# Kernel tuning notes

Hardware: AMD Instinct MI355X
Metric: run time of the kernel (lower is better)

## Reference

```python
import jax, jax.numpy as jnp
import numpy as np

N_NODES = 100000
N_EDGES = 1600000
IN_CH, HID, N_CLS = 768, 256, 8


def setup_inputs() -> dict:
    key = jax.random.key(0)
    k1, k2, k3, k4 = jax.random.split(key, 4)
    x = jax.random.normal(k1, (N_NODES, IN_CH), dtype=jnp.float32)
    edge_index = jax.random.randint(k2, (2, N_EDGES), 0, N_NODES, dtype=jnp.int64)
    # Glorot-ish init scaled for stability
    W1 = jax.random.normal(k3, (IN_CH, HID), dtype=jnp.float32) * (1.0 / np.sqrt(IN_CH))
    b1 = jnp.zeros((HID,), dtype=jnp.float32)
    W2 = jax.random.normal(k4, (HID, N_CLS), dtype=jnp.float32) * (1.0 / np.sqrt(HID))
    b2 = jnp.zeros((N_CLS,), dtype=jnp.float32)
    return {"x": x, "edge_index": edge_index, "W1": W1, "b1": b1, "W2": W2, "b2": b2}


def _gcn_norm(edge_index, num_nodes):
    # Add self-loops (PyG GCNConv default) and compute symmetric normalization.
    loops = jnp.arange(num_nodes, dtype=edge_index.dtype)
    row = jnp.concatenate([edge_index[0], loops])  # source nodes
    col = jnp.concatenate([edge_index[1], loops])  # target nodes
    ones = jnp.ones(col.shape[0], dtype=jnp.float32)
    deg = jax.ops.segment_sum(ones, col, num_segments=num_nodes)
    dinv = jnp.where(deg > 0, jax.lax.rsqrt(deg), 0.0)
    norm = dinv[row] * dinv[col]  # [E + N]
    return row, col, norm


def _gcn_conv(x, row, col, norm, W, b):
    h = x @ W                      # [N, out] dense transform first (out <= in)
    msg = h[row] * norm[:, None]    # gather + scale, [E+N, out]
    agg = jax.ops.segment_sum(msg, col, num_segments=x.shape[0])  # scatter-add
    return agg + b


def reference(x, edge_index, W1, b1, W2, b2):
    row, col, norm = _gcn_norm(edge_index, x.shape[0])
    h = _gcn_conv(x, row, col, norm, W1, b1)
    h = jax.nn.relu(h)
    # dropout is identity at eval (training=False)
    out = _gcn_conv(h, row, col, norm, W2, b2)
    return out
```

## Files before the change

kernel.cpp:

```cpp
#include <hip/hip_runtime.h>


#define NN 100000
#define NE 1600000
#define INC 768
#define HID 256
#define NCLS 8
#define NBLK 391

typedef short bf16x8 __attribute__((ext_vector_type(8)));
typedef float f32x4 __attribute__((ext_vector_type(4)));

__device__ __forceinline__ unsigned short f2bf(float f) {
  unsigned int u = __float_as_uint(f);
  unsigned int r = (u + 0x7FFFu + ((u >> 16) & 1u)) >> 16;
  return (unsigned short)r;
}
__device__ __forceinline__ float bf2f(unsigned short h) {
  return __uint_as_float(((unsigned int)h) << 16);
}

__global__ __launch_bounds__(256) void k_count(const int* __restrict__ ei, int* __restrict__ cnt) {
  int e = blockIdx.x * 256 + threadIdx.x;
  if (e < NE) atomicAdd(&cnt[ei[NE + e]], 1);
}

__global__ __launch_bounds__(256) void k_scan1(const int* __restrict__ cnt, int* __restrict__ bsum,
                                               float* __restrict__ dinv) {
  __shared__ int s[256];
  int i = blockIdx.x * 256 + threadIdx.x;
  int v = (i < NN) ? cnt[i] : 0;
  if (i < NN) dinv[i] = rsqrtf((float)v + 1.0f);
  s[threadIdx.x] = v;
  __syncthreads();
#pragma unroll
  for (int off = 128; off > 0; off >>= 1) {
    if (threadIdx.x < off) s[threadIdx.x] += s[threadIdx.x + off];
    __syncthreads();
  }
  if (threadIdx.x == 0) bsum[blockIdx.x] = s[0];
}
__global__ __launch_bounds__(512) void k_scan2(const int* __restrict__ bsum, int* __restrict__ boff,
                                               int* __restrict__ rowptr) {
  __shared__ int s[512];
  int tid = threadIdx.x;
  int v = (tid < NBLK) ? bsum[tid] : 0;
  s[tid] = v;
  __syncthreads();
#pragma unroll
  for (int off = 1; off < 512; off <<= 1) {
    int t = (tid >= off) ? s[tid - off] : 0;
    __syncthreads();
    s[tid] += t;
    __syncthreads();
  }
  if (tid < NBLK) boff[tid] = s[tid] - v;
  if (tid == NBLK - 1) rowptr[NN] = s[tid];
}
__global__ __launch_bounds__(256) void k_scan3(const int* __restrict__ cnt, const int* __restrict__ boff,
                                               int* __restrict__ rowptr, int* __restrict__ cursor) {
  __shared__ int s[256];
  int i = blockIdx.x * 256 + threadIdx.x;
  int v = (i < NN) ? cnt[i] : 0;
  s[threadIdx.x] = v;
  __syncthreads();
#pragma unroll
  for (int off = 1; off < 256; off <<= 1) {
    int t = (threadIdx.x >= off) ? s[threadIdx.x - off] : 0;
    __syncthreads();
    s[threadIdx.x] += t;
    __syncthreads();
  }
  if (i < NN) {
    int e = boff[blockIdx.x] + s[threadIdx.x] - v;
    rowptr[i] = e;
    cursor[i] = e;
  }
}
__global__ __launch_bounds__(256) void k_fill(const int* __restrict__ ei, const float* __restrict__ dinv,
                                              int* __restrict__ cursor, int2* __restrict__ epk) {
  int e = blockIdx.x * 256 + threadIdx.x;
  if (e >= NE) return;
  int r = ei[e];
  int c = ei[NE + e];
  float w = dinv[r] * dinv[c];
  int pos = atomicAdd(&cursor[c], 1);
  epk[pos] = make_int2(r, __float_as_int(w));
}

__global__ __launch_bounds__(256) void k_w1t(const float* __restrict__ W1, unsigned short* __restrict__ w1t) {
  int t = blockIdx.x * 256 + threadIdx.x;
  if (t >= INC * HID) return;
  int k = t / HID, n = t % HID;
  w1t[n * INC + k] = f2bf(W1[t]);
}

__global__ __launch_bounds__(512) void k_gemm1(const float* __restrict__ x,
                                               const unsigned short* __restrict__ w1t,
                                               unsigned short* __restrict__ h1) {
  __shared__ char smem[49152];
  unsigned short* As = (unsigned short*)smem;
  unsigned short* Bs = (unsigned short*)(smem + 16384);
  const int tid = threadIdx.x;
  const int lane = tid & 63;
  const int wid = tid >> 6;
  const int wm = wid >> 2;
  const int wn = wid & 3;
  const long bm = blockIdx.x;

  const int ar0 = tid >> 3, as7 = tid & 7;
  const int ar1 = (tid + 512) >> 3;
  long arow0 = bm * 128 + ar0; if (arow0 > NN - 1) arow0 = NN - 1;
  long arow1 = bm * 128 + ar1; if (arow1 > NN - 1) arow1 = NN - 1;
  const float* gA0 = x + arow0 * INC + as7 * 8;
  const float* gA1 = x + arow1 * INC + as7 * 8;
  const int aoff0 = (ar0 << 7) | ((as7 ^ (ar0 & 7)) << 4);
  const int aoff1 = (ar1 << 7) | ((as7 ^ (ar1 & 7)) << 4);

  f32x4 acc[4][4];
#pragma unroll
  for (int m = 0; m < 4; m++)
#pragma unroll
    for (int n = 0; n < 4; n++) acc[m][n] = (f32x4){0.f, 0.f, 0.f, 0.f};

  float4 fa00, fa01, fa10, fa11;
  uint4 rb0, rb1, rb2, rb3;

#define LOAD_AB(KT)                                                        \
  do {                                                                     \
    fa00 = *(const float4*)(gA0 + (KT));                                   \
    fa01 = *(const float4*)(gA0 + (KT) + 4);                               \
    fa10 = *(const float4*)(gA1 + (KT));                                   \
    fa11 = *(const float4*)(gA1 + (KT) + 4);                               \
    rb0 = *(const uint4*)(w1t + (long)(tid >> 3) * INC + (KT) + (tid & 7) * 8);            \
    rb1 = *(const uint4*)(w1t + (long)((tid + 512) >> 3) * INC + (KT) + (tid & 7) * 8);    \
    rb2 = *(const uint4*)(w1t + (long)((tid + 1024) >> 3) * INC + (KT) + (tid & 7) * 8);   \
    rb3 = *(const uint4*)(w1t + (long)((tid + 1536) >> 3) * INC + (KT) + (tid & 7) * 8);   \
  } while (0)

  LOAD_AB(0);

  for (int kt = 0; kt < INC; kt += 64) {
    {
      union { unsigned short us[8]; uint4 v; } u;
      u.us[0] = f2bf(fa00.x); u.us[1] = f2bf(fa00.y); u.us[2] = f2bf(fa00.z); u.us[3] = f2bf(fa00.w);
      u.us[4] = f2bf(fa01.x); u.us[5] = f2bf(fa01.y); u.us[6] = f2bf(fa01.z); u.us[7] = f2bf(fa01.w);
      *(uint4*)((char*)As + aoff0) = u.v;
      u.us[0] = f2bf(fa10.x); u.us[1] = f2bf(fa10.y); u.us[2] = f2bf(fa10.z); u.us[3] = f2bf(fa10.w);
      u.us[4] = f2bf(fa11.x); u.us[5] = f2bf(fa11.y); u.us[6] = f2bf(fa11.z); u.us[7] = f2bf(fa11.w);
      *(uint4*)((char*)As + aoff1) = u.v;
    }
    {
      int r0 = tid >> 3, s7 = tid & 7;
      *(uint4*)((char*)Bs + ((r0 << 7) | ((s7 ^ (r0 & 7)) << 4))) = rb0;
      int r1 = (tid + 512) >> 3;
      *(uint4*)((char*)Bs + ((r1 << 7) | ((s7 ^ (r1 & 7)) << 4))) = rb1;
      int r2 = (tid + 1024) >> 3;
      *(uint4*)((char*)Bs + ((r2 << 7) | ((s7 ^ (r2 & 7)) << 4))) = rb2;
      int r3 = (tid + 1536) >> 3;
      *(uint4*)((char*)Bs + ((r3 << 7) | ((s7 ^ (r3 & 7)) << 4))) = rb3;
    }
    __syncthreads();
    if (kt + 64 < INC) LOAD_AB(kt + 64);
#pragma unroll
    for (int half = 0; half < 2; half++) {
      bf16x8 af[4], bff[4];
      int j = (half << 2) + (lane >> 4);
#pragma unroll
      for (int m = 0; m < 4; m++) {
        int row = wm * 64 + m * 16 + (lane & 15);
        int off = (row << 7) | ((j ^ (row & 7)) << 4);
        af[m] = *(const bf16x8*)((const char*)As + off);
      }
#pragma unroll
      for (int n = 0; n < 4; n++) {
        int row = wn * 64 + n * 16 + (lane & 15);
        int off = (row << 7) | ((j ^ (row & 7)) << 4);
        bff[n] = *(const bf16x8*)((const char*)Bs + off);
      }
#pragma unroll
      for (int m = 0; m < 4; m++)
#pragma unroll
        for (int n = 0; n < 4; n++)
          acc[m][n] = __builtin_amdgcn_mfma_f32_16x16x32_bf16(af[m], bff[n], acc[m][n], 0, 0, 0);
    }
    __syncthreads();
  }
#undef LOAD_AB

  unsigned short* Os = (unsigned short*)smem;
#pragma unroll
  for (int chunk = 0; chunk < 2; chunk++) {
    if (wm == chunk) {
#pragma unroll
      for (int m = 0; m < 4; m++)
#pragma unroll
        for (int n = 0; n < 4; n++) {
          int lrow = m * 16 + ((lane >> 4) << 2);
          int lcol = wn * 64 + n * 16 + (lane & 15);
#pragma unroll
          for (int r = 0; r < 4; r++)
            Os[(lrow + r) * 264 + lcol] = f2bf(acc[m][n][r]);
        }
    }
    __syncthreads();
    {
      int r = tid >> 3, s = tid & 7;
      long grow = bm * 128 + chunk * 64 + r;
      if (grow < NN) {
        unsigned short* dst = h1 + grow * HID;
#pragma unroll
        for (int i = 0; i < 4; i++) {
          int seg = s + i * 8;
          *(uint4*)(dst + seg * 8) = *(const uint4*)((const char*)Os + (long)r * 528 + seg * 16);
        }
      }
    }
    __syncthreads();
  }
}

__global__ __launch_bounds__(256) void k_agg1(const unsigned short* __restrict__ h1,
                                              const float* __restrict__ dinv,
                                              const int* __restrict__ rowptr,
                                              const int2* __restrict__ epk,
                                              const float* __restrict__ b1,
                                              const float* __restrict__ W2,
                                              float* __restrict__ h2) {
  int w = (int)((blockIdx.x * 256 + threadIdx.x) >> 6);
  int lane = threadIdx.x & 63;
  if (w >= NN) return;
  float di = dinv[w];
  int c4 = lane << 2;
  const unsigned short* hb = h1 + c4;
  ushort4 hv = *(const ushort4*)(hb + (long)w * HID);
  float self = di * di;
  float a0 = self * bf2f(hv.x), a1 = self * bf2f(hv.y);
  float a2 = self * bf2f(hv.z), a3 = self * bf2f(hv.w);
  int e = rowptr[w], e1 = rowptr[w + 1];
  if ((e & 1) && e < e1) {
    int2 q = epk[e];
    float ws = __int_as_float(q.y);
    ushort4 g = *(const ushort4*)(hb + (long)q.x * HID);
    a0 += ws * bf2f(g.x); a1 += ws * bf2f(g.y);
    a2 += ws * bf2f(g.z); a3 += ws * bf2f(g.w);
    e++;
  }
  for (; e + 8 <= e1; e += 8) {
    uint4 p0 = *(const uint4*)(epk + e);
    uint4 p1 = *(const uint4*)(epk + e + 2);
    uint4 p2 = *(const uint4*)(epk + e + 4);
    uint4 p3 = *(const uint4*)(epk + e + 6);
    ushort4 g0 = *(const ushort4*)(hb + (long)(int)p0.x * HID);
    ushort4 g1 = *(const ushort4*)(hb + (long)(int)p0.z * HID);
    ushort4 g2 = *(const ushort4*)(hb + (long)(int)p1.x * HID);
    ushort4 g3 = *(const ushort4*)(hb + (long)(int)p1.z * HID);
    ushort4 g4 = *(const ushort4*)(hb + (long)(int)p2.x * HID);
    ushort4 g5 = *(const ushort4*)(hb + (long)(int)p2.z * HID);
    ushort4 g6 = *(const ushort4*)(hb + (long)(int)p3.x * HID);
    ushort4 g7 = *(const ushort4*)(hb + (long)(int)p3.z * HID);
    float w0 = __uint_as_float(p0.y), w1 = __uint_as_float(p0.w);
    float w2 = __uint_as_float(p1.y), w3 = __uint_as_float(p1.w);
    float w4 = __uint_as_float(p2.y), w5 = __uint_as_float(p2.w);
    float w6 = __uint_as_float(p3.y), w7 = __uint_as_float(p3.w);
    a0 += w0 * bf2f(g0.x) + w1 * bf2f(g1.x) + w2 * bf2f(g2.x) + w3 * bf2f(g3.x) +
          w4 * bf2f(g4.x) + w5 * bf2f(g5.x) + w6 * bf2f(g6.x) + w7 * bf2f(g7.x);
    a1 += w0 * bf2f(g0.y) + w1 * bf2f(g1.y) + w2 * bf2f(g2.y) + w3 * bf2f(g3.y) +
          w4 * bf2f(g4.y) + w5 * bf2f(g5.y) + w6 * bf2f(g6.y) + w7 * bf2f(g7.y);
    a2 += w0 * bf2f(g0.z) + w1 * bf2f(g1.z) + w2 * bf2f(g2.z) + w3 * bf2f(g3.z) +
          w4 * bf2f(g4.z) + w5 * bf2f(g5.z) + w6 * bf2f(g6.z) + w7 * bf2f(g7.z);
    a3 += w0 * bf2f(g0.w) + w1 * bf2f(g1.w) + w2 * bf2f(g2.w) + w3 * bf2f(g3.w) +
          w4 * bf2f(g4.w) + w5 * bf2f(g5.w) + w6 * bf2f(g6.w) + w7 * bf2f(g7.w);
  }
  for (; e + 2 <= e1; e += 2) {
    uint4 p = *(const uint4*)(epk + e);
    ushort4 g0 = *(const ushort4*)(hb + (long)(int)p.x * HID);
    ushort4 g1 = *(const ushort4*)(hb + (long)(int)p.z * HID);
    float w0 = __uint_as_float(p.y), w1 = __uint_as_float(p.w);
    a0 += w0 * bf2f(g0.x) + w1 * bf2f(g1.x);
    a1 += w0 * bf2f(g0.y) + w1 * bf2f(g1.y);
    a2 += w0 * bf2f(g0.z) + w1 * bf2f(g1.z);
    a3 += w0 * bf2f(g0.w) + w1 * bf2f(g1.w);
  }
  if (e < e1) {
    int2 q = epk[e];
    float ws = __int_as_float(q.y);
    ushort4 g = *(const ushort4*)(hb + (long)q.x * HID);
    a0 += ws * bf2f(g.x); a1 += ws * bf2f(g.y);
    a2 += ws * bf2f(g.z); a3 += ws * bf2f(g.w);
  }
  float4 bv = *(const float4*)(b1 + c4);
  float v0 = a0 + bv.x; v0 = v0 > 0.f ? v0 : 0.f;
  float v1 = a1 + bv.y; v1 = v1 > 0.f ? v1 : 0.f;
  float v2 = a2 + bv.z; v2 = v2 > 0.f ? v2 : 0.f;
  float v3 = a3 + bv.w; v3 = v3 > 0.f ? v3 : 0.f;
  const float4* wp = (const float4*)(W2 + ((long)c4 << 3));
  float4 r0a = wp[0], r0b = wp[1], r1a = wp[2], r1b = wp[3];
  float4 r2a = wp[4], r2b = wp[5], r3a = wp[6], r3b = wp[7];
  float p[8];
  p[0] = v0 * r0a.x + v1 * r1a.x + v2 * r2a.x + v3 * r3a.x;
  p[1] = v0 * r0a.y + v1 * r1a.y + v2 * r2a.y + v3 * r3a.y;
  p[2] = v0 * r0a.z + v1 * r1a.z + v2 * r2a.z + v3 * r3a.z;
  p[3] = v0 * r0a.w + v1 * r1a.w + v2 * r2a.w + v3 * r3a.w;
  p[4] = v0 * r0b.x + v1 * r1b.x + v2 * r2b.x + v3 * r3b.x;
  p[5] = v0 * r0b.y + v1 * r1b.y + v2 * r2b.y + v3 * r3b.y;
  p[6] = v0 * r0b.z + v1 * r1b.z + v2 * r2b.z + v3 * r3b.z;
  p[7] = v0 * r0b.w + v1 * r1b.w + v2 * r2b.w + v3 * r3b.w;
#pragma unroll
  for (int c = 0; c < 8; c++)
#pragma unroll
    for (int off = 1; off < 64; off <<= 1) p[c] += __shfl_xor(p[c], off, 64);
  if (lane < 8) {
    float o = p[0];
    o = (lane == 1) ? p[1] : o;
    o = (lane == 2) ? p[2] : o;
    o = (lane == 3) ? p[3] : o;
    o = (lane == 4) ? p[4] : o;
    o = (lane == 5) ? p[5] : o;
    o = (lane == 6) ? p[6] : o;
    o = (lane == 7) ? p[7] : o;
    h2[(long)w * NCLS + lane] = o;
  }
}

__global__ __launch_bounds__(256) void k_agg2(const float* __restrict__ h2,
                                              const float* __restrict__ dinv,
                                              const int* __restrict__ rowptr,
                                              const int2* __restrict__ epk,
                                              const float* __restrict__ b2,
                                              float* __restrict__ out) {
  long t = (long)blockIdx.x * 256 + threadIdx.x;
  long i = t >> 3;
  int c = (int)(t & 7);
  if (i >= NN) return;
  float di = dinv[i];
  float s = di * di * h2[i * NCLS + c];
  int e = rowptr[i], e1 = rowptr[i + 1];
  for (; e + 8 <= e1; e += 8) {
    int2 q0 = epk[e],     q1 = epk[e + 1], q2 = epk[e + 2], q3 = epk[e + 3];
    int2 q4 = epk[e + 4], q5 = epk[e + 5], q6 = epk[e + 6], q7 = epk[e + 7];
    float g0 = h2[(long)q0.x * NCLS + c], g1 = h2[(long)q1.x * NCLS + c];
    float g2 = h2[(long)q2.x * NCLS + c], g3 = h2[(long)q3.x * NCLS + c];
    float g4 = h2[(long)q4.x * NCLS + c], g5 = h2[(long)q5.x * NCLS + c];
    float g6 = h2[(long)q6.x * NCLS + c], g7 = h2[(long)q7.x * NCLS + c];
    s += __int_as_float(q0.y) * g0 + __int_as_float(q1.y) * g1 +
         __int_as_float(q2.y) * g2 + __int_as_float(q3.y) * g3 +
         __int_as_float(q4.y) * g4 + __int_as_float(q5.y) * g5 +
         __int_as_float(q6.y) * g6 + __int_as_float(q7.y) * g7;
  }
  for (; e < e1; e++) {
    int2 q = epk[e];
    s += __int_as_float(q.y) * h2[(long)q.x * NCLS + c];
  }
  out[i * NCLS + c] = s + b2[c];
}

extern "C" void kernel_launch(void* const* d_in, const int* in_sizes, int n_in,
                              void* d_out, int out_size, void* d_ws, size_t ws_size,
                              hipStream_t stream) {
  (void)in_sizes; (void)n_in; (void)out_size; (void)ws_size;
  const float* x  = (const float*)d_in[0];
  const int*   ei = (const int*)d_in[1];
  const float* W1 = (const float*)d_in[2];
  const float* b1 = (const float*)d_in[3];
  const float* W2 = (const float*)d_in[4];
  const float* b2 = (const float*)d_in[5];
  float* out = (float*)d_out;
  char* ws = (char*)d_ws;

  unsigned short* h1   = (unsigned short*)(ws + 0L);
  float* h2            = (float*)(ws + 51200000L);
  float* dinv          = (float*)(ws + 54400000L);
  int*   cnt           = (int*)(ws + 54800000L);
  int*   rowptr        = (int*)(ws + 55200000L);
  int*   cursor        = (int*)(ws + 55600128L);
  int2*  epk           = (int2*)(ws + 56000128L);
  unsigned short* w1t  = (unsigned short*)(ws + 68800128L);
  int*   bsum          = (int*)(ws + 69195008L);
  int*   boff          = (int*)(ws + 69196608L);

  hipMemsetAsync(cnt, 0, NN * sizeof(int), stream);
  k_count<<<(NE + 255) / 256, 256, 0, stream>>>(ei, cnt);
  k_scan1<<<NBLK, 256, 0, stream>>>(cnt, bsum, dinv);
  k_scan2<<<1, 512, 0, stream>>>(bsum, boff, rowptr);
  k_scan3<<<NBLK, 256, 0, stream>>>(cnt, boff, rowptr, cursor);
  k_fill<<<(NE + 255) / 256, 256, 0, stream>>>(ei, dinv, cursor, epk);
  k_w1t<<<(INC * HID + 255) / 256, 256, 0, stream>>>(W1, w1t);
  k_gemm1<<<782, 512, 0, stream>>>(x, w1t, h1);
  k_agg1<<<(NN * 64 + 255) / 256, 256, 0, stream>>>(h1, dinv, rowptr, epk, b1, W2, h2);
  k_agg2<<<(NN * NCLS + 255) / 256, 256, 0, stream>>>(h2, dinv, rowptr, epk, b2, out);
}
```

Baseline: 458.0 us.

## Fuse CSR fill into GEMM launch, deepen A prefetch, shrink agg1 blocks

Merges the edge-fill kernel into the GEMM launch as extra blocks so the atomic CSR fill can run concurrently with the dense GEMM and one launch disappears. The GEMM gets a two-stage A-register prefetch (two k-tiles in flight) and a launch-bounds occupancy hint of 4. The agg1 kernel moves from 256 to 128 threads per block. The costs are higher register pressure in the GEMM and fill blocks that each reserve 48KB of shared memory despite not using it.

```diff
diff --git a/kernel.cpp b/kernel.cpp
--- a/kernel.cpp
+++ b/kernel.cpp
@@ -7,6 +7,8 @@
 #define HID 256
 #define NCLS 8
 #define NBLK 391
+#define GEMMB 782
+#define FILLB 3125
 
 typedef short bf16x8 __attribute__((ext_vector_type(8)));
 typedef float f32x4 __attribute__((ext_vector_type(4)));
@@ -77,16 +79,6 @@
     cursor[i] = e;
   }
 }
-__global__ __launch_bounds__(256) void k_fill(const int* __restrict__ ei, const float* __restrict__ dinv,
-                                              int* __restrict__ cursor, int2* __restrict__ epk) {
-  int e = blockIdx.x * 256 + threadIdx.x;
-  if (e >= NE) return;
-  int r = ei[e];
-  int c = ei[NE + e];
-  float w = dinv[r] * dinv[c];
-  int pos = atomicAdd(&cursor[c], 1);
-  epk[pos] = make_int2(r, __float_as_int(w));
-}
 
 __global__ __launch_bounds__(256) void k_w1t(const float* __restrict__ W1, unsigned short* __restrict__ w1t) {
   int t = blockIdx.x * 256 + threadIdx.x;
@@ -95,10 +87,25 @@
   w1t[n * INC + k] = f2bf(W1[t]);
 }
 
-__global__ __launch_bounds__(512) void k_gemm1(const float* __restrict__ x,
-                                               const unsigned short* __restrict__ w1t,
-                                               unsigned short* __restrict__ h1) {
+__global__ __launch_bounds__(512, 4) void k_gemm_fill(const float* __restrict__ x,
+                                                      const unsigned short* __restrict__ w1t,
+                                                      unsigned short* __restrict__ h1,
+                                                      const int* __restrict__ ei,
+                                                      const float* __restrict__ dinv,
+                                                      int* __restrict__ cursor,
+                                                      int2* __restrict__ epk) {
   __shared__ char smem[49152];
+  if (blockIdx.x >= GEMMB) {
+    int e = (blockIdx.x - GEMMB) * 512 + threadIdx.x;
+    if (e < NE) {
+      int r = ei[e];
+      int c = ei[NE + e];
+      float w = dinv[r] * dinv[c];
+      int pos = atomicAdd(&cursor[c], 1);
+      epk[pos] = make_int2(r, __float_as_int(w));
+    }
+    return;
+  }
   unsigned short* As = (unsigned short*)smem;
   unsigned short* Bs = (unsigned short*)(smem + 16384);
   const int tid = threadIdx.x;
@@ -123,70 +130,97 @@
 #pragma unroll
     for (int n = 0; n < 4; n++) acc[m][n] = (f32x4){0.f, 0.f, 0.f, 0.f};
 
-  float4 fa00, fa01, fa10, fa11;
+  float4 Pa, Pb, Pc, Pd, Qa, Qb, Qc, Qd;
   uint4 rb0, rb1, rb2, rb3;
 
-#define LOAD_AB(KT)                                                        \
-  do {                                                                     \
-    fa00 = *(const float4*)(gA0 + (KT));                                   \
-    fa01 = *(const float4*)(gA0 + (KT) + 4);                               \
-    fa10 = *(const float4*)(gA1 + (KT));                                   \
-    fa11 = *(const float4*)(gA1 + (KT) + 4);                               \
+#define LOAD_ASET(Va, Vb, Vc, Vd, KT)             \
+  do {                                            \
+    Va = *(const float4*)(gA0 + (KT));            \
+    Vb = *(const float4*)(gA0 + (KT) + 4);        \
+    Vc = *(const float4*)(gA1 + (KT));            \
+    Vd = *(const float4*)(gA1 + (KT) + 4);        \
+  } while (0)
+#define LOAD_B(KT)                                                                         \
+  do {                                                                                     \
     rb0 = *(const uint4*)(w1t + (long)(tid >> 3) * INC + (KT) + (tid & 7) * 8);            \
     rb1 = *(const uint4*)(w1t + (long)((tid + 512) >> 3) * INC + (KT) + (tid & 7) * 8);    \
     rb2 = *(const uint4*)(w1t + (long)((tid + 1024) >> 3) * INC + (KT) + (tid & 7) * 8);   \
     rb3 = *(const uint4*)(w1t + (long)((tid + 1536) >> 3) * INC + (KT) + (tid & 7) * 8);   \
   } while (0)
-
-  LOAD_AB(0);
-
-  for (int kt = 0; kt < INC; kt += 64) {
-    {
-      union { unsigned short us[8]; uint4 v; } u;
-      u.us[0] = f2bf(fa00.x); u.us[1] = f2bf(fa00.y); u.us[2] = f2bf(fa00.z); u.us[3] = f2bf(fa00.w);
-      u.us[4] = f2bf(fa01.x); u.us[5] = f2bf(fa01.y); u.us[6] = f2bf(fa01.z); u.us[7] = f2bf(fa01.w);
-      *(uint4*)((char*)As + aoff0) = u.v;
-      u.us[0] = f2bf(fa10.x); u.us[1] = f2bf(fa10.y); u.us[2] = f2bf(fa10.z); u.us[3] = f2bf(fa10.w);
-      u.us[4] = f2bf(fa11.x); u.us[5] = f2bf(fa11.y); u.us[6] = f2bf(fa11.z); u.us[7] = f2bf(fa11.w);
-      *(uint4*)((char*)As + aoff1) = u.v;
-    }
-    {
-      int r0 = tid >> 3, s7 = tid & 7;
-      *(uint4*)((char*)Bs + ((r0 << 7) | ((s7 ^ (r0 & 7)) << 4))) = rb0;
-      int r1 = (tid + 512) >> 3;
-      *(uint4*)((char*)Bs + ((r1 << 7) | ((s7 ^ (r1 & 7)) << 4))) = rb1;
-      int r2 = (tid + 1024) >> 3;
-      *(uint4*)((char*)Bs + ((r2 << 7) | ((s7 ^ (r2 & 7)) << 4))) = rb2;
-      int r3 = (tid + 1536) >> 3;
-      *(uint4*)((char*)Bs + ((r3 << 7) | ((s7 ^ (r3 & 7)) << 4))) = rb3;
-    }
-    __syncthreads();
-    if (kt + 64 < INC) LOAD_AB(kt + 64);
-#pragma unroll
-    for (int half = 0; half < 2; half++) {
-      bf16x8 af[4], bff[4];
-      int j = (half << 2) + (lane >> 4);
-#pragma unroll
-      for (int m = 0; m < 4; m++) {
-        int row = wm * 64 + m * 16 + (lane & 15);
-        int off = (row << 7) | ((j ^ (row & 7)) << 4);
-        af[m] = *(const bf16x8*)((const char*)As + off);
-      }
-#pragma unroll
-      for (int n = 0; n < 4; n++) {
-        int row = wn * 64 + n * 16 + (lane & 15);
-        int off = (row << 7) | ((j ^ (row & 7)) << 4);
-        bff[n] = *(const bf16x8*)((const char*)Bs + off);
-      }
-#pragma unroll
-      for (int m = 0; m < 4; m++)
-#pragma unroll
-        for (int n = 0; n < 4; n++)
-          acc[m][n] = __builtin_amdgcn_mfma_f32_16x16x32_bf16(af[m], bff[n], acc[m][n], 0, 0, 0);
-    }
-    __syncthreads();
-  }
-#undef LOAD_AB
+#define WRITE_ASET(Va, Vb, Vc, Vd)                                                         \
+  do {                                                                                     \
+    union { unsigned short us[8]; uint4 v; } u;                                            \
+    u.us[0] = f2bf(Va.x); u.us[1] = f2bf(Va.y); u.us[2] = f2bf(Va.z);                      \
+    u.us[3] = f2bf(Va.w); u.us[4] = f2bf(Vb.x); u.us[5] = f2bf(Vb.y);                      \
+    u.us[6] = f2bf(Vb.z); u.us[7] = f2bf(Vb.w);                                            \
+    *(uint4*)((char*)As + aoff0) = u.v;                                                    \
+    u.us[0] = f2bf(Vc.x); u.us[1] = f2bf(Vc.y); u.us[2] = f2bf(Vc.z);                      \
+    u.us[3] = f2bf(Vc.w); u.us[4] = f2bf(Vd.x); u.us[5] = f2bf(Vd.y);                      \
+    u.us[6] = f2bf(Vd.z); u.us[7] = f2bf(Vd.w);                                            \
+    *(uint4*)((char*)As + aoff1) = u.v;                                                    \
+  } while (0)
+#define WRITE_B()                                                                          \
+  do {                                                                                     \
+    int r0 = tid >> 3, s7 = tid & 7;                                                       \
+    *(uint4*)((char*)Bs + ((r0 << 7) | ((s7 ^ (r0 & 7)) << 4))) = rb0;                     \
+    int r1 = (tid + 512) >> 3;                                                             \
+    *(uint4*)((char*)Bs + ((r1 << 7) | ((s7 ^ (r1 & 7)) << 4))) = rb1;                     \
+    int r2 = (tid + 1024) >> 3;                                                            \
+    *(uint4*)((char*)Bs + ((r2 << 7) | ((s7 ^ (r2 & 7)) << 4))) = rb2;                     \
+    int r3 = (tid + 1536) >> 3;                                                            \
+    *(uint4*)((char*)Bs + ((r3 << 7) | ((s7 ^ (r3 & 7)) << 4))) = rb3;                     \
+  } while (0)
+#define MFMA_STEP()                                                                        \
+  do {                                                                                     \
+    _Pragma("unroll")                                                                      \
+    for (int half = 0; half < 2; half++) {                                                 \
+      bf16x8 af[4], bff[4];                                                                \
+      int j = (half << 2) + (lane >> 4);                                                   \
+      _Pragma("unroll")                                                                    \
+      for (int m = 0; m < 4; m++) {                                                        \
+        int row = wm * 64 + m * 16 + (lane & 15);                                          \
+        af[m] = *(const bf16x8*)((const char*)As + ((row << 7) | ((j ^ (row & 7)) << 4))); \
+      }                                                                                    \
+      _Pragma("unroll")                                                                    \
+      for (int n = 0; n < 4; n++) {                                                        \
+        int row = wn * 64 + n * 16 + (lane & 15);                                          \
+        bff[n] = *(const bf16x8*)((const char*)Bs + ((row << 7) | ((j ^ (row & 7)) << 4)));\
+      }                                                                                    \
+      _Pragma("unroll")                                                                    \
+      for (int m = 0; m < 4; m++)                                                          \
+        _Pragma("unroll")                                                                  \
+        for (int n = 0; n < 4; n++)                                                        \
+          acc[m][n] = __builtin_amdgcn_mfma_f32_16x16x32_bf16(af[m], bff[n], acc[m][n], 0, 0, 0); \
+    }                                                                                      \
+  } while (0)
+
+  LOAD_ASET(Pa, Pb, Pc, Pd, 0);
+  LOAD_B(0);
+  LOAD_ASET(Qa, Qb, Qc, Qd, 64);
+
+#pragma unroll 1
+  for (int u = 0; u < 6; u++) {
+    int kt = u * 128;
+    WRITE_ASET(Pa, Pb, Pc, Pd);
+    WRITE_B();
+    __syncthreads();
+    if (kt + 64 < INC) LOAD_B(kt + 64);
+    if (kt + 128 < INC) LOAD_ASET(Pa, Pb, Pc, Pd, kt + 128);
+    MFMA_STEP();
+    __syncthreads();
+    WRITE_ASET(Qa, Qb, Qc, Qd);
+    WRITE_B();
+    __syncthreads();
+    if (kt + 128 < INC) LOAD_B(kt + 128);
+    if (kt + 192 < INC) LOAD_ASET(Qa, Qb, Qc, Qd, kt + 192);
+    MFMA_STEP();
+    __syncthreads();
+  }
+#undef LOAD_ASET
+#undef LOAD_B
+#undef WRITE_ASET
+#undef WRITE_B
+#undef MFMA_STEP
 
   unsigned short* Os = (unsigned short*)smem;
 #pragma unroll
@@ -220,14 +254,14 @@
   }
 }
 
-__global__ __launch_bounds__(256) void k_agg1(const unsigned short* __restrict__ h1,
+__global__ __launch_bounds__(128) void k_agg1(const unsigned short* __restrict__ h1,
                                               const float* __restrict__ dinv,
                                               const int* __restrict__ rowptr,
                                               const int2* __restrict__ epk,
                                               const float* __restrict__ b1,
                                               const float* __restrict__ W2,
                                               float* __restrict__ h2) {
-  int w = (int)((blockIdx.x * 256 + threadIdx.x) >> 6);
+  int w = (int)((blockIdx.x * 128 + threadIdx.x) >> 6);
   int lane = threadIdx.x & 63;
   if (w >= NN) return;
   float di = dinv[w];
@@ -384,9 +418,8 @@
   k_scan1<<<NBLK, 256, 0, stream>>>(cnt, bsum, dinv);
   k_scan2<<<1, 512, 0, stream>>>(bsum, boff, rowptr);
   k_scan3<<<NBLK, 256, 0, stream>>>(cnt, boff, rowptr, cursor);
-  k_fill<<<(NE + 255) / 256, 256, 0, stream>>>(ei, dinv, cursor, epk);
   k_w1t<<<(INC * HID + 255) / 256, 256, 0, stream>>>(W1, w1t);
-  k_gemm1<<<782, 512, 0, stream>>>(x, w1t, h1);
-  k_agg1<<<(NN * 64 + 255) / 256, 256, 0, stream>>>(h1, dinv, rowptr, epk, b1, W2, h2);
+  k_gemm_fill<<<GEMMB + FILLB, 512, 0, stream>>>(x, w1t, h1, ei, dinv, cursor, epk);
+  k_agg1<<<(NN * 64 + 127) / 128, 128, 0, stream>>>(h1, dinv, rowptr, epk, b1, W2, h2);
   k_agg2<<<(NN * NCLS + 255) / 256, 256, 0, stream>>>(h2, dinv, rowptr, epk, b2, out);
 }
```

After: 779.6 us. 1.7x slower.
